# Kernel optimization log

Measured on AMD Instinct MI355X. Metric: run time of the kernel, lower is better.

Reference implementation:

```python
import jax, jax.numpy as jnp
import numpy as np

DIM = 2048
H = 16
DK = DIM // H   # head_k = 128
DV = DIM // H   # head_v = 128
B = 4
N = 4096
INV_SQRT_DK = 1.0 / float(np.sqrt(DK))


def setup_inputs() -> dict:
    key = jax.random.key(0)
    ks = jax.random.split(key, 12)
    s = 0.02
    return {
        "x": jax.random.normal(ks[0], (B, N, DIM), dtype=jnp.float32),
        "M_fast_prev": jax.random.normal(ks[1], (B, H, DK, DV), dtype=jnp.float32) * 0.05,
        "M_slow_prev": jax.random.normal(ks[2], (B, H, DK, DV), dtype=jnp.float32) * 0.05,
        "Wq": jax.random.normal(ks[3], (DIM, H * DK), dtype=jnp.float32) * s,
        "Wk": jax.random.normal(ks[4], (DIM, H * DK), dtype=jnp.float32) * s,
        "Wv": jax.random.normal(ks[5], (DIM, H * DV), dtype=jnp.float32) * s,
        "Wo": jax.random.normal(ks[6], (H * DV, DIM), dtype=jnp.float32) * s,
        "W_bilinear": jax.random.normal(ks[7], (H, DK, DK), dtype=jnp.float32) * 0.02,
        "fast_slope": jnp.full((H, 1, 1), 0.5, dtype=jnp.float32),
        "slow_slope": jnp.full((H, 1, 1), 0.01, dtype=jnp.float32),
        "inter_fast": jnp.full((H, 1, 1), 0.1, dtype=jnp.float32),
        "inter_slow": jnp.full((H, 1, 1), 0.9, dtype=jnp.float32),
        "S_fast": jax.random.normal(ks[8], (H, DK, DK), dtype=jnp.float32) * 0.05,
        "S_slow": jax.random.normal(ks[9], (H, DK, DK), dtype=jnp.float32) * 0.02,
        "f1_w": jax.random.normal(ks[10], (DIM, DIM // 2), dtype=jnp.float32) * s,
        "f1_b": jnp.zeros((DIM // 2,), dtype=jnp.float32),
        "f2_w": jax.random.normal(ks[11], (DIM // 2, H), dtype=jnp.float32) * s,
        "f2_b": jnp.zeros((H,), dtype=jnp.float32),
    }


def reference(x, M_fast_prev, M_slow_prev, Wq, Wk, Wv, Wo, W_bilinear,
              fast_slope, slow_slope, inter_fast, inter_slow,
              S_fast, S_slow, f1_w, f1_b, f2_w, f2_b):
    b, n, _ = x.shape
    # projections -> [b, h, n, d]
    q = (x @ Wq).reshape(b, n, H, DK).transpose(0, 2, 1, 3)
    k = (x @ Wk).reshape(b, n, H, DK).transpose(0, 2, 1, 3)
    v = (x @ Wv).reshape(b, n, H, DV).transpose(0, 2, 1, 3)

    # bilinear resonance modulation of keys
    resonance = jnp.tanh(jnp.einsum('bhnd,hde->bhne', k, W_bilinear))
    k_mod = k * (1.0 + 0.5 * resonance) * INV_SQRT_DK

    # exponential fast/slow decay weights over positions: [h, n, 1]
    idx = (jnp.arange(n, dtype=x.dtype) - (n - 1))[:, None]  # [n, 1]
    fast_w = jnp.exp(fast_slope * idx)  # [h, n, 1]
    slow_w = jnp.exp(slow_slope * idx)

    k_fast = k_mod * fast_w[None]  # [b, h, n, dk]
    k_slow = k_mod * slow_w[None]

    # outer-product state accumulation: [b, h, dk, dv]
    M_fast_curr = jnp.einsum('bhnd,bhnv->bhdv', k_fast, v)
    M_slow_curr = jnp.einsum('bhnd,bhnv->bhdv', k_slow, v)

    # inter-block state carry
    M_fast = M_fast_prev * inter_fast[None] + M_fast_curr
    M_slow = M_slow_prev * inter_slow[None] + M_slow_curr

    # refinement: (I + S) @ M
    eye = jnp.eye(DK, dtype=x.dtype)
    Mf_ref = jnp.einsum('hde,bhev->bhdv', eye[None] + S_fast, M_fast)
    Ms_ref = jnp.einsum('hde,bhev->bhdv', eye[None] + S_slow, M_slow)

    o_fast = jnp.einsum('bhnd,bhdv->bhnv', q, Mf_ref)
    o_slow = jnp.einsum('bhnd,bhdv->bhnv', q, Ms_ref)

    # flux gating from pooled tokens
    h1 = jax.nn.silu(x.mean(axis=1) @ f1_w + f1_b)
    psi = jax.nn.sigmoid(h1 @ f2_w + f2_b)  # [b, h]
    pe = psi[:, :, None, None]

    o_blend = (1.0 - pe) * o_fast + pe * o_slow  # [b, h, n, dv]
    o_blend = o_blend.transpose(0, 2, 1, 3).reshape(b, n, H * DV)
    out = o_blend @ Wo
    return out, M_fast, M_slow, psi
```

## Files before the change

kernel.cpp:

```cpp
#include <hip/hip_runtime.h>
#include <math.h>

typedef __bf16 bf16;
typedef __attribute__((ext_vector_type(8))) __bf16 bf16x8;
typedef __attribute__((ext_vector_type(4))) __bf16 bf16x4;
typedef __attribute__((ext_vector_type(2))) __bf16 bf16x2;
typedef __attribute__((ext_vector_type(4))) float f32x4;

#define DIM 2048
#define NH 16
#define DKK 128
#define BATCH 4
#define SEQ 4096
#define BN (BATCH*SEQ)
#define INV_SQRT_DK 0.08838834764831845f

#define MFMA16(a,b,c) __builtin_amdgcn_mfma_f32_16x16x32_bf16((a),(b),(c),0,0,0)

#define GLDS(gp, lp) __builtin_amdgcn_global_load_lds( \
    (const __attribute__((address_space(1))) void*)(gp), \
    (__attribute__((address_space(3))) void*)(lp), 16, 0, 0)

__device__ inline void stage_tile(const bf16* __restrict__ g, int ld,
                                  bf16* lds, int lane, int wave) {
  const int rl = lane >> 3;
  const int gc = ((lane & 7) ^ (rl & 7)) << 3;
  const bf16* gp = g + (size_t)(wave * 32 + rl) * ld + gc;
#pragma unroll
  for (int t = 0; t < 4; ++t)
    GLDS(gp + (size_t)(t * 8) * ld, lds + (wave * 32 + t * 8) * 64);
}

__device__ inline bf16x8 frag8(const bf16* lds, int r, int kc) {
  return *(const bf16x8*)(lds + r * 64 + (((kc ^ (r & 7)) << 3)));
}

__device__ inline void stage_sq(const bf16* __restrict__ g, bf16* lds, int lane, int wave) {
  const int rl = lane >> 4;
  const int lc = lane & 15;
#pragma unroll
  for (int t = 0; t < 8; ++t) {
    int r = wave * 32 + t * 4 + rl;
    int gc = (lc ^ (r & 7)) << 3;
    GLDS(g + (size_t)r * 128 + gc, lds + (wave * 32 + t * 4) * 128);
  }
}
__device__ inline bf16x8 frag8w(const bf16* lds, int r, int kc) {
  return *(const bf16x8*)(lds + r * 128 + (((kc ^ (r & 7)) << 3)));
}
__device__ inline int sqaddr(int r, int c) {
  return r * 128 + ((((c >> 3) ^ (r & 7)) << 3) | (c & 7));
}

__device__ inline float fast_exp(float x) { return __expf(x); }
__device__ inline float fast_tanh(float x) {
  float e2 = __expf(2.f * x);
  return 1.f - 2.f / (e2 + 1.f);
}

__global__ __launch_bounds__(256) void conv_bf16(const float* __restrict__ x,
                                                 bf16* __restrict__ y) {
  int i = (blockIdx.x * 256 + threadIdx.x) * 4;
  float4 v = *(const float4*)(x + i);
  bf16x4 o = { (bf16)v.x, (bf16)v.y, (bf16)v.z, (bf16)v.w };
  *(bf16x4*)(y + i) = o;
}

__global__ __launch_bounds__(256) void tconv4(const float* W0, const float* W1,
                                              const float* W2, const float* W3,
                                              bf16* O0, bf16* O1, bf16* O2, bf16* O3) {
  __shared__ float tile[32][33];
  const float* Wp; bf16* Op;
  switch (blockIdx.z) {
    case 0: Wp = W0; Op = O0; break;
    case 1: Wp = W1; Op = O1; break;
    case 2: Wp = W2; Op = O2; break;
    default: Wp = W3; Op = O3; break;
  }
  int c0 = blockIdx.x * 32, r0 = blockIdx.y * 32;
  int tx = threadIdx.x, ty = threadIdx.y;
#pragma unroll
  for (int i = 0; i < 4; ++i)
    tile[ty + i*8][tx] = Wp[(size_t)(r0 + ty + i*8) * DIM + c0 + tx];
  __syncthreads();
#pragma unroll
  for (int i = 0; i < 4; ++i)
    Op[(size_t)(c0 + ty + i*8) * DIM + r0 + tx] = (bf16)tile[tx][ty + i*8];
}

__global__ __launch_bounds__(256) void tconvWb(const float* __restrict__ W,
                                               bf16* __restrict__ Wt) {
  __shared__ float tile[32][33];
  const float* Wp = W + (size_t)blockIdx.z * DKK * DKK;
  bf16* Wtp = Wt + (size_t)blockIdx.z * DKK * DKK;
  int c0 = blockIdx.x * 32, r0 = blockIdx.y * 32;
  int tx = threadIdx.x, ty = threadIdx.y;
#pragma unroll
  for (int i = 0; i < 4; ++i)
    tile[ty + i*8][tx] = Wp[(size_t)(r0 + ty + i*8) * DKK + c0 + tx];
  __syncthreads();
#pragma unroll
  for (int i = 0; i < 4; ++i)
    Wtp[(size_t)(c0 + ty + i*8) * DKK + r0 + tx] = (bf16)tile[tx][ty + i*8];
}

__global__ __launch_bounds__(256) void rweights(const float* __restrict__ fs,
                                                const float* __restrict__ ss,
                                                float* __restrict__ rbuf) {
  int n = blockIdx.x * 256 + threadIdx.x;
  int h = blockIdx.y;
  rbuf[h * SEQ + n] = fast_exp((fs[h] - ss[h]) * (float)(n - (SEQ - 1)));
}

__global__ void zero_f32(float* p, int n) {
  int i = blockIdx.x * 256 + threadIdx.x;
  if (i < n) p[i] = 0.f;
}

__global__ __launch_bounds__(256) void mean_part(const bf16* __restrict__ xb,
                                                 float* __restrict__ xm) {
  int d0 = (blockIdx.x * 256 + threadIdx.x) * 2;
  int b = blockIdx.z;
  const bf16* xp = xb + ((size_t)b * SEQ + (size_t)blockIdx.y * 256) * DIM + d0;
  float s0 = 0.f, s1 = 0.f;
#pragma unroll 8
  for (int n = 0; n < 256; ++n) {
    bf16x2 v = *(const bf16x2*)(xp + (size_t)n * DIM);
    s0 += (float)v[0]; s1 += (float)v[1];
  }
  atomicAdd(&xm[b * DIM + d0], s0);
  atomicAdd(&xm[b * DIM + d0 + 1], s1);
}

__global__ __launch_bounds__(256) void mlp1(const float* __restrict__ xm,
                                            const float* __restrict__ f1w,
                                            float* __restrict__ h1raw) {
  int j = blockIdx.x * 256 + threadIdx.x;
  int b = blockIdx.y;
  int k0 = blockIdx.z * 256;
  const float* xmb = xm + b * DIM + k0;
  const float* w = f1w + (size_t)k0 * (DIM/2) + j;
  float s = 0.f;
#pragma unroll 4
  for (int k = 0; k < 256; ++k) s += xmb[k] * w[(size_t)k * (DIM/2)];
  atomicAdd(&h1raw[b * (DIM/2) + j], s);
}

__global__ void mlp2(const float* __restrict__ h1raw,
                     const float* __restrict__ f1b,
                     const float* __restrict__ f2w,
                     const float* __restrict__ f2b,
                     float* __restrict__ psi_out) {
  int t = threadIdx.x;
  int b = t >> 4, h = t & 15;
  float s = f2b[h];
  for (int k = 0; k < DIM/2; ++k) {
    float hv = h1raw[b * (DIM/2) + k] * (1.f / (float)SEQ) + f1b[k];
    hv = hv / (1.f + fast_exp(-hv));
    s += hv * f2w[k * NH + h];
  }
  psi_out[t] = 1.f / (1.f + fast_exp(-s));
}

template<int MODE>
__global__ __launch_bounds__(256) void gemm_bt(const bf16* __restrict__ A, int lda,
                                               const bf16* __restrict__ Bt, int ldb,
                                               void* __restrict__ Cv, int ldc, int K) {
  __shared__ bf16 sA[128 * 64];
  __shared__ bf16 sB[128 * 64];
  const int tid = threadIdx.x;
  const int lane = tid & 63;
  const int wave = tid >> 6;
  const int quad = lane >> 4;
  const int wm = (wave & 1) * 64;
  const int wn = (wave >> 1) * 64;
  const size_t m0 = (size_t)blockIdx.y * 128;
  const size_t n0 = (size_t)blockIdx.x * 128;
  f32x4 acc[4][4] = {};
  for (int k0 = 0; k0 < K; k0 += 64) {
    stage_tile(A + m0 * lda + k0, lda, sA, lane, wave);
    stage_tile(Bt + n0 * ldb + k0, ldb, sB, lane, wave);
    __syncthreads();
#pragma unroll
    for (int kk = 0; kk < 2; ++kk) {
      const int kc = kk * 4 + quad;
      bf16x8 af[4], bfr[4];
#pragma unroll
      for (int i = 0; i < 4; ++i) af[i] = frag8(sA, wm + i*16 + (lane & 15), kc);
#pragma unroll
      for (int j = 0; j < 4; ++j) bfr[j] = frag8(sB, wn + j*16 + (lane & 15), kc);
#pragma unroll
      for (int i = 0; i < 4; ++i)
#pragma unroll
        for (int j = 0; j < 4; ++j)
          acc[i][j] = MFMA16(af[i], bfr[j], acc[i][j]);
    }
    __syncthreads();
  }
  if (MODE == 2) {
    const int h = (int)(n0 >> 7) & (NH - 1);
    const int b = (int)(m0 >> 12);
    const int nbase0 = (int)(m0 & 4095) + wm + quad * 4;
    bf16* vt = (bf16*)Cv;
#pragma unroll
    for (int i = 0; i < 4; ++i)
#pragma unroll
      for (int j = 0; j < 4; ++j) {
        int dv = wn + j*16 + (lane & 15);
        bf16x4 p = { (bf16)acc[i][j][0], (bf16)acc[i][j][1],
                     (bf16)acc[i][j][2], (bf16)acc[i][j][3] };
        *(bf16x4*)(vt + ((size_t)(b * NH + h) * DKK + dv) * SEQ + nbase0 + i * 16) = p;
      }
  } else {
#pragma unroll
    for (int i = 0; i < 4; ++i)
#pragma unroll
      for (int j = 0; j < 4; ++j) {
        size_t col = n0 + wn + j*16 + (lane & 15);
        size_t row = m0 + wm + i*16 + quad * 4;
#pragma unroll
        for (int r = 0; r < 4; ++r) {
          if (MODE == 1) ((float*)Cv)[(row + r) * ldc + col] = acc[i][j][r];
          else           ((bf16*)Cv)[(row + r) * ldc + col] = (bf16)acc[i][j][r];
        }
      }
  }
}

__global__ __launch_bounds__(256) void gemm_k_res(const bf16* __restrict__ xb,
                                                  const bf16* __restrict__ Wtk,
                                                  const bf16* __restrict__ Wbt,
                                                  const float* __restrict__ slow_slope,
                                                  bf16* __restrict__ kts) {
  __shared__ bf16 smem[2 * 128 * 128];
  bf16* sA = smem;
  bf16* sB = smem + 8192;
  bf16* K2 = smem;
  bf16* W2 = smem + 16384;
  const int tid = threadIdx.x;
  const int lane = tid & 63;
  const int wave = tid >> 6;
  const int quad = lane >> 4;
  const int wm = (wave & 1) * 64;
  const int wn = (wave >> 1) * 64;
  const int h = blockIdx.x;
  const size_t m0 = (size_t)blockIdx.y * 128;
  const int b = (int)(m0 >> 12);
  const int bh = b * NH + h;
  const float ss = slow_slope[h];

  stage_sq(Wbt + (size_t)h * DKK * DKK, W2, lane, wave);

  const bf16* Ap = xb + m0 * DIM;
  const bf16* Bp = Wtk + (size_t)h * 128 * DIM;
  f32x4 acc[4][4] = {};
  for (int k0 = 0; k0 < DIM; k0 += 64) {
    stage_tile(Ap + k0, DIM, sA, lane, wave);
    stage_tile(Bp + k0, DIM, sB, lane, wave);
    __syncthreads();
#pragma unroll
    for (int kk = 0; kk < 2; ++kk) {
      const int kc = kk * 4 + quad;
      bf16x8 af[4], bfr[4];
#pragma unroll
      for (int i = 0; i < 4; ++i) af[i] = frag8(sA, wm + i*16 + (lane & 15), kc);
#pragma unroll
      for (int j = 0; j < 4; ++j) bfr[j] = frag8(sB, wn + j*16 + (lane & 15), kc);
#pragma unroll
      for (int i = 0; i < 4; ++i)
#pragma unroll
        for (int j = 0; j < 4; ++j)
          acc[i][j] = MFMA16(af[i], bfr[j], acc[i][j]);
    }
    __syncthreads();
  }
#pragma unroll
  for (int i = 0; i < 4; ++i)
#pragma unroll
    for (int j = 0; j < 4; ++j) {
      int c = wn + j*16 + (lane & 15);
#pragma unroll
      for (int r = 0; r < 4; ++r) {
        int row = wm + i*16 + quad*4 + r;
        K2[sqaddr(row, c)] = (bf16)acc[i][j][r];
      }
    }
  __syncthreads();
  f32x4 accR[4][4] = {};
#pragma unroll
  for (int kk = 0; kk < 4; ++kk) {
    const int kc = kk * 4 + quad;
    bf16x8 af[4], bfr[4];
#pragma unroll
    for (int i = 0; i < 4; ++i) af[i] = frag8w(K2, wm + i*16 + (lane & 15), kc);
#pragma unroll
    for (int j = 0; j < 4; ++j) bfr[j] = frag8w(W2, wn + j*16 + (lane & 15), kc);
#pragma unroll
    for (int i = 0; i < 4; ++i)
#pragma unroll
      for (int j = 0; j < 4; ++j)
        accR[i][j] = MFMA16(af[i], bfr[j], accR[i][j]);
  }
  float wsv[4][4];
#pragma unroll
  for (int i = 0; i < 4; ++i)
#pragma unroll
    for (int r = 0; r < 4; ++r) {
      int nseq = (int)(m0 & 4095) + wm + i*16 + quad*4 + r;
      wsv[i][r] = fast_exp(ss * (float)(nseq - (SEQ - 1)));
    }
#pragma unroll
  for (int i = 0; i < 4; ++i)
#pragma unroll
    for (int j = 0; j < 4; ++j) {
      int c = wn + j*16 + (lane & 15);
      bf16x4 p;
#pragma unroll
      for (int r = 0; r < 4; ++r) {
        int row = wm + i*16 + quad*4 + r;
        float kv = (float)K2[sqaddr(row, c)];
        float res = fast_tanh(accR[i][j][r]);
        p[r] = (bf16)(kv * (1.f + 0.5f * res) * INV_SQRT_DK * wsv[i][r]);
      }
      int nbase = (int)(m0 & 4095) + wm + i*16 + quad*4;
      *(bf16x4*)(kts + ((size_t)bh * DKK + c) * SEQ + nbase) = p;
    }
}

__global__ __launch_bounds__(256) void mcurr(const bf16* __restrict__ kts,
                                             const bf16* __restrict__ vt,
                                             const float* __restrict__ rbuf,
                                             float* __restrict__ partials) {
  __shared__ bf16 sK[128 * 64];
  __shared__ bf16 sV[128 * 64];
  const int tid = threadIdx.x;
  const int lane = tid & 63;
  const int wave = tid >> 6;
  const int quad = lane >> 4;
  const int wm = (wave & 1) * 64, wn = (wave >> 1) * 64;
  const int s = blockIdx.x;
  const int bh = blockIdx.y;
  const int h = bh & (NH - 1);
  const bf16* Ap = kts + (size_t)bh * DKK * SEQ;
  const bf16* Bp = vt + (size_t)bh * DKK * SEQ;
  const float* rp = rbuf + (size_t)h * SEQ;
  f32x4 accF[4][4] = {}, accS[4][4] = {};
  for (int k0 = s * 512; k0 < s * 512 + 512; k0 += 64) {
    stage_tile(Ap + k0, SEQ, sK, lane, wave);
    stage_tile(Bp + k0, SEQ, sV, lane, wave);
    __syncthreads();
#pragma unroll
    for (int kk = 0; kk < 2; ++kk) {
      const int kc = kk * 4 + quad;
      const int kn = k0 + kc * 8;
      float rv[8];
      *(f32x4*)rv       = *(const f32x4*)(rp + kn);
      *(f32x4*)(rv + 4) = *(const f32x4*)(rp + kn + 4);
      bf16x8 afS[4], afF[4], bfv[4];
#pragma unroll
      for (int i = 0; i < 4; ++i) afS[i] = frag8(sK, wm + i*16 + (lane & 15), kc);
#pragma unroll
      for (int j = 0; j < 4; ++j) bfv[j] = frag8(sV, wn + j*16 + (lane & 15), kc);
#pragma unroll
      for (int i = 0; i < 4; ++i)
#pragma unroll
        for (int e = 0; e < 8; ++e)
          afF[i][e] = (bf16)((float)afS[i][e] * rv[e]);
#pragma unroll
      for (int i = 0; i < 4; ++i)
#pragma unroll
        for (int j = 0; j < 4; ++j) {
          accS[i][j] = MFMA16(afS[i], bfv[j], accS[i][j]);
          accF[i][j] = MFMA16(afF[i], bfv[j], accF[i][j]);
        }
    }
    __syncthreads();
  }
  float* Pf = partials + ((size_t)(s * 64 + bh) * 2 + 0) * (DKK * DKK);
  float* Ps = partials + ((size_t)(s * 64 + bh) * 2 + 1) * (DKK * DKK);
#pragma unroll
  for (int i = 0; i < 4; ++i)
#pragma unroll
    for (int j = 0; j < 4; ++j) {
      int col = wn + j*16 + (lane & 15);
      int row = wm + i*16 + quad * 4;
#pragma unroll
      for (int r = 0; r < 4; ++r) {
        Pf[(row + r) * DKK + col] = accF[i][j][r];
        Ps[(row + r) * DKK + col] = accS[i][j][r];
      }
    }
}

__global__ __launch_bounds__(256) void finalize(const float* __restrict__ partials,
                                                const float* __restrict__ Mf_prev,
                                                const float* __restrict__ Ms_prev,
                                                const float* __restrict__ inter_fast,
                                                const float* __restrict__ inter_slow,
                                                const float* __restrict__ S_fast,
                                                const float* __restrict__ S_slow,
                                                const float* __restrict__ psi,
                                                float* __restrict__ Mf_out,
                                                float* __restrict__ Ms_out,
                                                bf16* __restrict__ Mbt) {
  __shared__ float sMf[128 * 33];
  __shared__ float sMs[128 * 33];
  const int t = threadIdx.x;
  const int bh = blockIdx.x;
  const int h = bh & (NH - 1);
  const int e0 = blockIdx.y * 32;
  const int el = t & 31;
  const int d0 = t >> 5;
  const float inf_ = inter_fast[h], ins_ = inter_slow[h];
  const size_t mb = (size_t)bh * (DKK * DKK);
#pragma unroll
  for (int i = 0; i < 16; ++i) {
    int d = d0 + 8 * i;
    int g = d * DKK + e0 + el;
    float mf = inf_ * Mf_prev[mb + g];
    float ms = ins_ * Ms_prev[mb + g];
#pragma unroll
    for (int s = 0; s < 8; ++s) {
      mf += partials[((size_t)(s * 64 + bh) * 2 + 0) * (DKK*DKK) + g];
      ms += partials[((size_t)(s * 64 + bh) * 2 + 1) * (DKK*DKK) + g];
    }
    Mf_out[mb + g] = mf;
    Ms_out[mb + g] = ms;
    sMf[d * 33 + el] = mf;
    sMs[d * 33 + el] = ms;
  }
  __syncthreads();
  const float p = psi[bh];
  for (int i = 0; i < 16; ++i) {
    int d = d0 + 8 * i;
    float accf = sMf[d * 33 + el];
    float accs = sMs[d * 33 + el];
    const float* Sf = S_fast + (size_t)h * (DKK*DKK) + (size_t)d * DKK;
    const float* Ss = S_slow + (size_t)h * (DKK*DKK) + (size_t)d * DKK;
    for (int k = 0; k < DKK; ++k) {
      accf += Sf[k] * sMf[k * 33 + el];
      accs += Ss[k] * sMs[k * 33 + el];
    }
    float blend = (1.f - p) * accf + p * accs;
    Mbt[mb + (size_t)(e0 + el) * DKK + d] = (bf16)blend;
  }
}

__global__ __launch_bounds__(256) void o_gemm(const bf16* __restrict__ qb,
                                              const bf16* __restrict__ Mbt,
                                              bf16* __restrict__ ob) {
  __shared__ bf16 sA[128 * 64];
  __shared__ bf16 sB[128 * 64];
  const int tid = threadIdx.x;
  const int lane = tid & 63;
  const int wave = tid >> 6;
  const int quad = lane >> 4;
  const int wm = (wave & 1) * 64, wn = (wave >> 1) * 64;
  const int h = blockIdx.x;
  const int rc = blockIdx.y;
  const int b = rc >> 5;
  const int bh = b * NH + h;
  const bf16* Ap = qb + (size_t)rc * 128 * DIM + h * DKK;
  const bf16* Bp = Mbt + (size_t)bh * DKK * DKK;
  bf16* Cp = ob + (size_t)rc * 128 * DIM + h * DKK;
  f32x4 acc[4][4] = {};
#pragma unroll
  for (int k0 = 0; k0 < DKK; k0 += 64) {
    stage_tile(Ap + k0, DIM, sA, lane, wave);
    stage_tile(Bp + k0, DKK, sB, lane, wave);
    __syncthreads();
#pragma unroll
    for (int kk = 0; kk < 2; ++kk) {
      const int kc = kk * 4 + quad;
      bf16x8 af[4], bfr[4];
#pragma unroll
      for (int i = 0; i < 4; ++i) af[i] = frag8(sA, wm + i*16 + (lane & 15), kc);
#pragma unroll
      for (int j = 0; j < 4; ++j) bfr[j] = frag8(sB, wn + j*16 + (lane & 15), kc);
#pragma unroll
      for (int i = 0; i < 4; ++i)
#pragma unroll
        for (int j = 0; j < 4; ++j)
          acc[i][j] = MFMA16(af[i], bfr[j], acc[i][j]);
    }
    __syncthreads();
  }
#pragma unroll
  for (int i = 0; i < 4; ++i)
#pragma unroll
    for (int j = 0; j < 4; ++j) {
      int col = wn + j*16 + (lane & 15);
      int rowl = wm + i*16 + quad * 4;
#pragma unroll
      for (int r = 0; r < 4; ++r)
        Cp[(size_t)(rowl + r) * DIM + col] = (bf16)acc[i][j][r];
    }
}

extern "C" void kernel_launch(void* const* d_in, const int* in_sizes, int n_in,
                              void* d_out, int out_size, void* d_ws, size_t ws_size,
                              hipStream_t stream) {
  const float* x        = (const float*)d_in[0];
  const float* Mf_prev  = (const float*)d_in[1];
  const float* Ms_prev  = (const float*)d_in[2];
  const float* Wq       = (const float*)d_in[3];
  const float* Wk       = (const float*)d_in[4];
  const float* Wv       = (const float*)d_in[5];
  const float* Wo       = (const float*)d_in[6];
  const float* Wbil     = (const float*)d_in[7];
  const float* fast_slope = (const float*)d_in[8];
  const float* slow_slope = (const float*)d_in[9];
  const float* inter_fast = (const float*)d_in[10];
  const float* inter_slow = (const float*)d_in[11];
  const float* S_fast   = (const float*)d_in[12];
  const float* S_slow   = (const float*)d_in[13];
  const float* f1w      = (const float*)d_in[14];
  const float* f1b      = (const float*)d_in[15];
  const float* f2w      = (const float*)d_in[16];
  const float* f2b      = (const float*)d_in[17];

  char* ws = (char*)d_ws;
  bf16*  xb       = (bf16*)(ws);
  bf16*  qb       = (bf16*)(ws + 67108864);
  bf16*  Wtq      = (bf16*)(ws + 134217728);
  bf16*  Wtk      = (bf16*)(ws + 142606336);
  bf16*  Wtv      = (bf16*)(ws + 150994944);
  bf16*  Wto      = (bf16*)(ws + 159383552);
  bf16*  Wbt      = (bf16*)(ws + 167772160);
  float* rbuf     = (float*)(ws + 168296448);
  bf16*  Mbt      = (bf16*)(ws + 168558592);
  float* xm       = (float*)(ws + 170655744);
  float* h1raw    = (float*)(ws + 170688512);
  float* partials = (float*)ws;
  bf16*  ob       = (bf16*)ws;

  float* out  = (float*)d_out;
  float* MfO  = out + 33554432;
  float* MsO  = MfO + 1048576;
  float* psiO = MsO + 1048576;
  bf16* kts = (bf16*)d_out;
  bf16* vt  = kts + 33554432;

  conv_bf16<<<dim3(BN * DIM / 1024), 256, 0, stream>>>(x, xb);
  tconv4<<<dim3(64, 64, 4), dim3(32, 8), 0, stream>>>(Wq, Wk, Wv, Wo, Wtq, Wtk, Wtv, Wto);
  tconvWb<<<dim3(4, 4, NH), dim3(32, 8), 0, stream>>>(Wbil, Wbt);
  rweights<<<dim3(16, 16), 256, 0, stream>>>(fast_slope, slow_slope, rbuf);

  zero_f32<<<dim3(48), 256, 0, stream>>>(xm, BATCH * DIM + BATCH * (DIM/2));
  mean_part<<<dim3(4, 16, 4), 256, 0, stream>>>(xb, xm);
  mlp1<<<dim3(4, 4, 8), 256, 0, stream>>>(xm, f1w, h1raw);
  mlp2<<<dim3(1), 64, 0, stream>>>(h1raw, f1b, f2w, f2b, psiO);

  gemm_bt<0><<<dim3(16, 128), 256, 0, stream>>>(xb, DIM, Wtq, DIM, qb, DIM, DIM);
  gemm_bt<2><<<dim3(16, 128), 256, 0, stream>>>(xb, DIM, Wtv, DIM, vt, 0, DIM);
  gemm_k_res<<<dim3(16, 128), 256, 0, stream>>>(xb, Wtk, Wbt, slow_slope, kts);

  mcurr<<<dim3(8, 64), 256, 0, stream>>>(kts, vt, rbuf, partials);

  finalize<<<dim3(64, 4), 256, 0, stream>>>(partials, Mf_prev, Ms_prev, inter_fast,
                                            inter_slow, S_fast, S_slow, psiO,
                                            MfO, MsO, Mbt);

  o_gemm<<<dim3(NH, 128), 256, 0, stream>>>(qb, Mbt, ob);

  gemm_bt<1><<<dim3(16, 128), 256, 0, stream>>>(ob, DIM, Wto, DIM, out, DIM, DIM);
}
```

Measured before the change: 1.279 ms.

## Fold per-head state into output weights to skip o_gemm intermediate

Reassociates (q·M)·Wo as q·(M·Wo). A per-batch weight W2 = blockdiag(M_bh)·Wo is built by a small w2_gemm, and the final projection becomes one per-batch GEMM of q against W2, which removes the o_gemm pass and the write and re-read of the ob intermediate. The K-resonance kernel also stages W_bilinear in 64-column tiles to cut LDS use and so allow more occupancy. The cost is a 4×2048×2048 weight built per call, and the extra rounding of W2 to bf16 may change accuracy.

```diff
diff --git a/kernel.cpp b/kernel.cpp
--- a/kernel.cpp
+++ b/kernel.cpp
@@ -35,16 +35,6 @@
   return *(const bf16x8*)(lds + r * 64 + (((kc ^ (r & 7)) << 3)));
 }
 
-__device__ inline void stage_sq(const bf16* __restrict__ g, bf16* lds, int lane, int wave) {
-  const int rl = lane >> 4;
-  const int lc = lane & 15;
-#pragma unroll
-  for (int t = 0; t < 8; ++t) {
-    int r = wave * 32 + t * 4 + rl;
-    int gc = (lc ^ (r & 7)) << 3;
-    GLDS(g + (size_t)r * 128 + gc, lds + (wave * 32 + t * 4) * 128);
-  }
-}
 __device__ inline bf16x8 frag8w(const bf16* lds, int r, int kc) {
   return *(const bf16x8*)(lds + r * 128 + (((kc ^ (r & 7)) << 3)));
 }
@@ -176,10 +166,12 @@
   const int wn = (wave >> 1) * 64;
   const size_t m0 = (size_t)blockIdx.y * 128;
   const size_t n0 = (size_t)blockIdx.x * 128;
+  const bf16* Bp = Bt;
+  if (MODE == 3) Bp += (size_t)(m0 >> 12) * DIM * DIM;
   f32x4 acc[4][4] = {};
   for (int k0 = 0; k0 < K; k0 += 64) {
     stage_tile(A + m0 * lda + k0, lda, sA, lane, wave);
-    stage_tile(Bt + n0 * ldb + k0, ldb, sB, lane, wave);
+    stage_tile(Bp + n0 * ldb + k0, ldb, sB, lane, wave);
     __syncthreads();
 #pragma unroll
     for (int kk = 0; kk < 2; ++kk) {
@@ -220,7 +212,7 @@
         size_t row = m0 + wm + i*16 + quad * 4;
 #pragma unroll
         for (int r = 0; r < 4; ++r) {
-          if (MODE == 1) ((float*)Cv)[(row + r) * ldc + col] = acc[i][j][r];
+          if (MODE == 3) ((float*)Cv)[(row + r) * ldc + col] = acc[i][j][r];
           else           ((bf16*)Cv)[(row + r) * ldc + col] = (bf16)acc[i][j][r];
         }
       }
@@ -232,11 +224,11 @@
                                                   const bf16* __restrict__ Wbt,
                                                   const float* __restrict__ slow_slope,
                                                   bf16* __restrict__ kts) {
-  __shared__ bf16 smem[2 * 128 * 128];
+  __shared__ bf16 smem[3 * 128 * 64];
   bf16* sA = smem;
   bf16* sB = smem + 8192;
   bf16* K2 = smem;
-  bf16* W2 = smem + 16384;
+  bf16* sW = smem + 16384;
   const int tid = threadIdx.x;
   const int lane = tid & 63;
   const int wave = tid >> 6;
@@ -249,8 +241,6 @@
   const int bh = b * NH + h;
   const float ss = slow_slope[h];
 
-  stage_sq(Wbt + (size_t)h * DKK * DKK, W2, lane, wave);
-
   const bf16* Ap = xb + m0 * DIM;
   const bf16* Bp = Wtk + (size_t)h * 128 * DIM;
   f32x4 acc[4][4] = {};
@@ -287,19 +277,27 @@
     }
   __syncthreads();
   f32x4 accR[4][4] = {};
-#pragma unroll
-  for (int kk = 0; kk < 4; ++kk) {
-    const int kc = kk * 4 + quad;
-    bf16x8 af[4], bfr[4];
-#pragma unroll
-    for (int i = 0; i < 4; ++i) af[i] = frag8w(K2, wm + i*16 + (lane & 15), kc);
-#pragma unroll
-    for (int j = 0; j < 4; ++j) bfr[j] = frag8w(W2, wn + j*16 + (lane & 15), kc);
-#pragma unroll
-    for (int i = 0; i < 4; ++i)
-#pragma unroll
-      for (int j = 0; j < 4; ++j)
-        accR[i][j] = MFMA16(af[i], bfr[j], accR[i][j]);
+  const bf16* Wp = Wbt + (size_t)h * DKK * DKK;
+#pragma unroll
+  for (int k0 = 0; k0 < 128; k0 += 64) {
+    stage_tile(Wp + k0, DKK, sW, lane, wave);
+    __syncthreads();
+#pragma unroll
+    for (int kk = 0; kk < 2; ++kk) {
+      const int kcl = kk * 4 + quad;
+      const int kcg = (k0 >> 3) + kcl;
+      bf16x8 af[4], bfr[4];
+#pragma unroll
+      for (int i = 0; i < 4; ++i) af[i] = frag8w(K2, wm + i*16 + (lane & 15), kcg);
+#pragma unroll
+      for (int j = 0; j < 4; ++j) bfr[j] = frag8(sW, wn + j*16 + (lane & 15), kcl);
+#pragma unroll
+      for (int i = 0; i < 4; ++i)
+#pragma unroll
+        for (int j = 0; j < 4; ++j)
+          accR[i][j] = MFMA16(af[i], bfr[j], accR[i][j]);
+    }
+    __syncthreads();
   }
   float wsv[4][4];
 #pragma unroll
@@ -402,7 +400,7 @@
                                                 const float* __restrict__ psi,
                                                 float* __restrict__ Mf_out,
                                                 float* __restrict__ Ms_out,
-                                                bf16* __restrict__ Mbt) {
+                                                bf16* __restrict__ Mb) {
   __shared__ float sMf[128 * 33];
   __shared__ float sMs[128 * 33];
   const int t = threadIdx.x;
@@ -442,13 +440,13 @@
       accs += Ss[k] * sMs[k * 33 + el];
     }
     float blend = (1.f - p) * accf + p * accs;
-    Mbt[mb + (size_t)(e0 + el) * DKK + d] = (bf16)blend;
-  }
-}
-
-__global__ __launch_bounds__(256) void o_gemm(const bf16* __restrict__ qb,
-                                              const bf16* __restrict__ Mbt,
-                                              bf16* __restrict__ ob) {
+    Mb[mb + (size_t)d * DKK + e0 + el] = (bf16)blend;
+  }
+}
+
+__global__ __launch_bounds__(256) void w2_gemm(const bf16* __restrict__ Mb,
+                                               const bf16* __restrict__ Wto,
+                                               bf16* __restrict__ W2t) {
   __shared__ bf16 sA[128 * 64];
   __shared__ bf16 sB[128 * 64];
   const int tid = threadIdx.x;
@@ -456,18 +454,16 @@
   const int wave = tid >> 6;
   const int quad = lane >> 4;
   const int wm = (wave & 1) * 64, wn = (wave >> 1) * 64;
-  const int h = blockIdx.x;
-  const int rc = blockIdx.y;
-  const int b = rc >> 5;
-  const int bh = b * NH + h;
-  const bf16* Ap = qb + (size_t)rc * 128 * DIM + h * DKK;
-  const bf16* Bp = Mbt + (size_t)bh * DKK * DKK;
-  bf16* Cp = ob + (size_t)rc * 128 * DIM + h * DKK;
+  const int c0 = blockIdx.x * 128;
+  const int bh = blockIdx.y;
+  const int h = bh & (NH - 1), b = bh >> 4;
+  const bf16* Ap = Mb + (size_t)bh * DKK * DKK;
+  const bf16* Bp = Wto + (size_t)c0 * DIM + h * DKK;
   f32x4 acc[4][4] = {};
 #pragma unroll
   for (int k0 = 0; k0 < DKK; k0 += 64) {
-    stage_tile(Ap + k0, DIM, sA, lane, wave);
-    stage_tile(Bp + k0, DKK, sB, lane, wave);
+    stage_tile(Ap + k0, DKK, sA, lane, wave);
+    stage_tile(Bp + k0, DIM, sB, lane, wave);
     __syncthreads();
 #pragma unroll
     for (int kk = 0; kk < 2; ++kk) {
@@ -485,15 +481,16 @@
     }
     __syncthreads();
   }
+  bf16* base = W2t + (size_t)b * DIM * DIM + h * DKK;
 #pragma unroll
   for (int i = 0; i < 4; ++i)
 #pragma unroll
     for (int j = 0; j < 4; ++j) {
       int col = wn + j*16 + (lane & 15);
-      int rowl = wm + i*16 + quad * 4;
-#pragma unroll
-      for (int r = 0; r < 4; ++r)
-        Cp[(size_t)(rowl + r) * DIM + col] = (bf16)acc[i][j][r];
+      int row0 = wm + i*16 + quad * 4;
+      bf16x4 p = { (bf16)acc[i][j][0], (bf16)acc[i][j][1],
+                   (bf16)acc[i][j][2], (bf16)acc[i][j][3] };
+      *(bf16x4*)(base + (size_t)(c0 + col) * DIM + row0) = p;
     }
 }
 
@@ -528,11 +525,11 @@
   bf16*  Wto      = (bf16*)(ws + 159383552);
   bf16*  Wbt      = (bf16*)(ws + 167772160);
   float* rbuf     = (float*)(ws + 168296448);
-  bf16*  Mbt      = (bf16*)(ws + 168558592);
+  bf16*  Mb       = (bf16*)(ws + 168558592);
   float* xm       = (float*)(ws + 170655744);
   float* h1raw    = (float*)(ws + 170688512);
   float* partials = (float*)ws;
-  bf16*  ob       = (bf16*)ws;
+  bf16*  W2t      = (bf16*)ws;
 
   float* out  = (float*)d_out;
   float* MfO  = out + 33554432;
@@ -559,9 +556,9 @@
 
   finalize<<<dim3(64, 4), 256, 0, stream>>>(partials, Mf_prev, Ms_prev, inter_fast,
                                             inter_slow, S_fast, S_slow, psiO,
-                                            MfO, MsO, Mbt);
-
-  o_gemm<<<dim3(NH, 128), 256, 0, stream>>>(qb, Mbt, ob);
-
-  gemm_bt<1><<<dim3(16, 128), 256, 0, stream>>>(ob, DIM, Wto, DIM, out, DIM, DIM);
-}
+                                            MfO, MsO, Mb);
+
+  w2_gemm<<<dim3(16, 64), 256, 0, stream>>>(Mb, Wto, W2t);
+
+  gemm_bt<3><<<dim3(16, 128), 256, 0, stream>>>(qb, DIM, W2t, DIM, out, DIM, DIM);
+}
```

After: 1.281 ms. Within noise of the previous version (+0.1%).
